# Kernel tuning notes

Measured on AMD Instinct MI355X. Metric: run time of the kernel, lower is better.

Reference implementation:

```python
import jax, jax.numpy as jnp
import numpy as np

B, L, D, H, DH, S_POKES = 1, 4096, 1024, 16, 64, 3072


def setup_inputs() -> dict:
    key = jax.random.key(0)
    k0, k1, k2, k3 = jax.random.split(key, 4)
    x = jax.random.normal(k0, (B, L, D), jnp.float32)
    pos = jax.random.uniform(k1, (B, L, 2), jnp.float32)  # positions in [0,1]^2
    qkv_w = jax.random.normal(k2, (3 * D, D), jnp.float32) * 0.02
    out_w = jax.random.normal(k3, (D, D), jnp.float32) * 0.02
    scale = jnp.ones((H,), jnp.float32) * 10.0  # per-head cosine-sim scale (init 10)
    # AxialRoPE2D freq table: logspace(pi, 10*pi), view(2, d_head//4, n_heads).mT
    n = H * DH // 4
    f = np.exp(np.linspace(np.log(np.pi), np.log(10.0 * np.pi), n + 1)[:-1])
    freqs = jnp.asarray(np.stack([f, f]).reshape(2, DH // 4, H).transpose(0, 2, 1), jnp.float32)
    return {"x": x, "pos": pos, "qkv_w": qkv_w, "out_w": out_w,
            "scale": scale, "freqs": freqs, "n_pokes": S_POKES}


def _cos_scale(q, k, scale, eps=1e-8):
    # scale_for_cosine_sim: qk logits = scale * cosine_similarity
    sq = jnp.sum(q * q, axis=-1, keepdims=True)
    sk = jnp.sum(k * k, axis=-1, keepdims=True)
    ss = jnp.sqrt(jnp.abs(scale) + eps)
    return q * (ss * jax.lax.rsqrt(sq + eps)), k * (ss * jax.lax.rsqrt(sk + eps))


def _axial_theta(pos, freqs):
    # pos [B,L,2] in [0,1]; theta [B,H,L,DH//2]
    th_w = (pos[..., None, 0:1] * 2.0 - 1.0) * freqs[0]  # [B,L,H,DH//4]
    th_h = (pos[..., None, 1:2] * 2.0 - 1.0) * freqs[1]
    return jnp.concatenate([th_h, th_w], axis=-1).transpose(0, 2, 1, 3)


def _rope(x, theta):
    d = theta.shape[-1]  # DH//2 -> rotates the full head dim, x3 part empty
    x1, x2 = x[..., :d], x[..., d:2 * d]
    cos, sin = jnp.cos(theta), jnp.sin(theta)
    return jnp.concatenate([x1 * cos - x2 * sin, x2 * cos + x1 * sin], axis=-1)


def reference(x, pos, qkv_w, out_w, scale, freqs, n_pokes):
    b, l, dm = x.shape
    qkv = x @ qkv_w.T                          # [B,L,3D]
    q, k, v = jnp.split(qkv, 3, axis=-1)
    split_heads = lambda t: t.reshape(b, l, H, DH).transpose(0, 2, 1, 3)  # [B,H,L,DH]
    q, k, v = split_heads(q), split_heads(k), split_heads(v)
    q, k = _cos_scale(q, k, scale.reshape(1, H, 1, 1))
    theta = _axial_theta(pos, freqs)
    q, k = _rope(q, theta), _rope(k, theta)
    s = n_pokes
    qp, kp, vp = q[:, :, :s], k[:, :, :s], v[:, :, :s]
    qq, kq, vq = q[:, :, s:], k[:, :, s:], v[:, :, s:]
    # pokes: causal self-attention (scale=1.0, cosine-sim logits)
    sc_pp = jnp.einsum('bhqd,bhkd->bhqk', qp, kp)
    causal = jnp.tril(jnp.ones((s, s), bool))
    p_pp = jax.nn.softmax(jnp.where(causal, sc_pp, -jnp.inf), axis=-1)
    out_p = jnp.einsum('bhqk,bhkd->bhqd', p_pp, vp)
    # queries: attend to all pokes + themselves (diagonal), never each other
    sc_qp = jnp.einsum('bhqd,bhkd->bhqk', qq, kp)          # [B,H,Q,S]
    sc_self = jnp.sum(qq * kq, axis=-1, keepdims=True)     # [B,H,Q,1]
    p_q = jax.nn.softmax(jnp.concatenate([sc_qp, sc_self], axis=-1), axis=-1)
    out_q = jnp.einsum('bhqk,bhkd->bhqd', p_q[..., :s], vp) + p_q[..., s:] * vq
    out = jnp.concatenate([out_p, out_q], axis=2).transpose(0, 2, 1, 3).reshape(b, l, dm)
    return out @ out_w.T
```

## Files before the change

### kernel.cpp

```cpp
#include <hip/hip_runtime.h>
#include <math.h>

#define SEQL   4096
#define DMODEL 1024
#define NH     16
#define DHEAD  64
#define SPOKES 3072
#define NQUERY (SEQL - SPOKES)
#define QKVN   (3 * DMODEL)

typedef short bf16x8 __attribute__((ext_vector_type(8)));
typedef short bf16x4 __attribute__((ext_vector_type(4)));
typedef float f32x4  __attribute__((ext_vector_type(4)));

__device__ __forceinline__ short f2bf(float f) {
    unsigned u = __builtin_bit_cast(unsigned, f);
    u += 0x7fffu + ((u >> 16) & 1u);
    return (short)(u >> 16);
}
__device__ __forceinline__ float bf2f(short s) {
    unsigned u = ((unsigned)(unsigned short)s) << 16;
    return __builtin_bit_cast(float, u);
}
__device__ __forceinline__ unsigned cvt_pk_bf16(float lo, float hi) {
    unsigned u;
    asm("v_cvt_pk_bf16_f32 %0, %1, %2" : "=v"(u) : "v"(lo), "v"(hi));
    return u;
}
__device__ __forceinline__ int swz(int row) { return ((row & 7) ^ (row >> 3)) << 4; }

__device__ __forceinline__ void gload_lds16(const void* g, void* l) {
    __builtin_amdgcn_global_load_lds(
        (const __attribute__((address_space(1))) unsigned int*)g,
        (__attribute__((address_space(3))) unsigned int*)l,
        16, 0, 0);
}

__global__ __launch_bounds__(256) void cvt_f32_bf16(
    const float* __restrict__ in, short* __restrict__ out, int n8)
{
    const int i = blockIdx.x * 256 + threadIdx.x;
    if (i >= n8) return;
    float4 a = ((const float4*)in)[i * 2];
    float4 b = ((const float4*)in)[i * 2 + 1];
    bf16x8 v;
    v[0] = f2bf(a.x); v[1] = f2bf(a.y); v[2] = f2bf(a.z); v[3] = f2bf(a.w);
    v[4] = f2bf(b.x); v[5] = f2bf(b.y); v[6] = f2bf(b.z); v[7] = f2bf(b.w);
    ((bf16x8*)out)[i] = v;
}

template<bool BF16OUT>
__global__ __launch_bounds__(256) void gemm_bf16(
    const short* __restrict__ A, const short* __restrict__ B, void* __restrict__ Cv,
    int K, int ldc)
{
    __shared__ short As[128 * 64];
    __shared__ short Bs[128 * 64];

    const int t = threadIdx.x;
    const int lane = t & 63, w = t >> 6;
    const int c = lane & 15, g = lane >> 4;
    const int wr = w >> 1, wc = w & 1;
    const int m0 = blockIdx.y * 128, n0 = blockIdx.x * 128;

    f32x4 acc[4][4] = {};

    for (int k0 = 0; k0 < K; k0 += 64) {
        __syncthreads();
        #pragma unroll
        for (int i = 0; i < 4; ++i) {
            const int chunk = (w * 4 + i) * 64 + lane;
            const int row = chunk >> 3, cc = chunk & 7;
            gload_lds16(A + (size_t)(m0 + row) * K + k0 + cc * 8,
                        As + (size_t)(w * 4 + i) * 512);
            gload_lds16(B + (size_t)(n0 + row) * K + k0 + cc * 8,
                        Bs + (size_t)(w * 4 + i) * 512);
        }
        __syncthreads();

        #pragma unroll
        for (int kk = 0; kk < 2; ++kk) {
            bf16x8 af[4], bf[4];
            #pragma unroll
            for (int i = 0; i < 4; ++i)
                af[i] = *(const bf16x8*)(As + (wr * 64 + i * 16 + c) * 64 + kk * 32 + g * 8);
            #pragma unroll
            for (int j = 0; j < 4; ++j)
                bf[j] = *(const bf16x8*)(Bs + (wc * 64 + j * 16 + c) * 64 + kk * 32 + g * 8);
            #pragma unroll
            for (int i = 0; i < 4; ++i)
                #pragma unroll
                for (int j = 0; j < 4; ++j)
                    acc[i][j] = __builtin_amdgcn_mfma_f32_16x16x32_bf16(af[i], bf[j], acc[i][j], 0, 0, 0);
        }
    }

    #pragma unroll
    for (int i = 0; i < 4; ++i)
        #pragma unroll
        for (int r = 0; r < 4; ++r) {
            const int row = m0 + wr * 64 + i * 16 + g * 4 + r;
            #pragma unroll
            for (int j = 0; j < 4; ++j) {
                const int col = n0 + wc * 64 + j * 16 + c;
                const float v = acc[i][j][r];
                if (BF16OUT) ((short*)Cv)[(size_t)row * ldc + col] = f2bf(v);
                else         ((float*)Cv)[(size_t)row * ldc + col] = v;
            }
        }
}

__global__ __launch_bounds__(256) void transform_qk(
    short* __restrict__ qkv, const float* __restrict__ pos,
    const float* __restrict__ scale, const float* __restrict__ freqs)
{
    const int w    = threadIdx.x >> 6;
    const int lane = threadIdx.x & 63;
    const int rid  = blockIdx.x * 4 + w;
    const int l    = rid >> 4;
    const int h    = rid & 15;

    short* qp = qkv + (size_t)l * QKVN + h * DHEAD;
    short* kp = qp + DMODEL;

    float q = bf2f(qp[lane]);
    float k = bf2f(kp[lane]);

    float sq = q * q, sk = k * k;
    #pragma unroll
    for (int o = 32; o > 0; o >>= 1) {
        sq += __shfl_xor(sq, o);
        sk += __shfl_xor(sk, o);
    }
    const float ss = sqrtf(fabsf(scale[h]) + 1e-8f);
    q *= ss * rsqrtf(sq + 1e-8f);
    k *= ss * rsqrtf(sk + 1e-8f);

    const int   j  = lane & 31;
    const float p  = pos[l * 2 + (j < 16 ? 1 : 0)];
    const float fj = (j < 16) ? freqs[256 + h * 16 + j] : freqs[h * 16 + (j - 16)];
    const float th = (p * 2.0f - 1.0f) * fj;
    const float cs = cosf(th), sn = sinf(th);

    const float qo = __shfl_xor(q, 32);
    const float ko = __shfl_xor(k, 32);
    const float qr = (lane < 32) ? q * cs - qo * sn : q * cs + qo * sn;
    const float kr = (lane < 32) ? k * cs - ko * sn : k * cs + ko * sn;

    qp[lane] = f2bf(qr);
    kp[lane] = f2bf(kr);
}

__global__ __launch_bounds__(256) void attn_fused(
    const short* __restrict__ qkv, short* __restrict__ attn,
    short* __restrict__ pacc_c, float* __restrict__ pml_c, float* __restrict__ pml0_c,
    short* __restrict__ pacc_q, float* __restrict__ pml_q, float* __restrict__ pml0_q)
{
    __shared__ short Kl[64 * 64];
    __shared__ short VTl[64 * 64];
    __shared__ short Pl[4][16 * 64];

    const int h = blockIdx.y;
    const int t = threadIdx.x, lane = t & 63, w = t >> 6;
    const int c = lane & 15, g = lane >> 4;
    const int qcol = h * DHEAD, kcol = DMODEL + h * DHEAD, vcol = 2 * DMODEL + h * DHEAD;

    const int xc = blockIdx.x;
    bool causal; int z, NS, q0, kt0, ktn, qt = 0, qb = 0;
    if (xc < 48) {
        causal = false; qb = xc / 3; z = xc - qb * 3; NS = 3;
        q0 = SPOKES + qb * 64; kt0 = z * 16; ktn = 16;
    } else {
        causal = true;
        if (xc < 96)       { const int i = xc - 48; qt = 47 - i / 3; z = i - (i / 3) * 3; NS = 3; }
        else if (xc < 128) { const int i = xc - 96; qt = 31 - (i >> 1); z = i & 1; NS = 2; }
        else               { qt = 143 - xc; z = 0; NS = 1; }
        q0 = qt * 64;
        const int full = qt + 1, b = full / NS, r = full - b * NS;
        kt0 = z * b + (z < r ? z : r);
        ktn = b + (z < r ? 1 : 0);
    }

    const int qg = q0 + w * 16 + c;

    bf16x8 qf0, qf1;
    {
        const short* qrow = qkv + (size_t)qg * QKVN + qcol;
        qf0 = *(const bf16x8*)(qrow + g * 8);
        qf1 = *(const bf16x8*)(qrow + 32 + g * 8);
    }

    float m = -INFINITY, l = 0.0f;
    f32x4 acc[4] = {};
    bf16x8 vregA, vregB;

    auto KDMA = [&](int kt) {
        const int k0 = kt * 64;
        #pragma unroll
        for (int i = 0; i < 2; ++i) {
            const int ch = i * 256 + t;
            const int kv = ch >> 3, s = ch & 7;
            const int o = s ^ ((kv & 7) ^ (kv >> 3));
            gload_lds16(qkv + (size_t)(k0 + kv) * QKVN + kcol + o * 8,
                        (char*)Kl + i * 4096 + w * 1024);
        }
    };
    auto VLOAD = [&](int kt) {
        const int k0 = kt * 64;
        const short* v0 = qkv + (size_t)(k0 + 2 * (t >> 3)) * QKVN + vcol + (t & 7) * 8;
        vregA = *(const bf16x8*)v0;
        vregB = *(const bf16x8*)(v0 + QKVN);
    };
    auto VWRITE = [&]() {
        const int p2 = t >> 3, oc = t & 7;
        #pragma unroll
        for (int j = 0; j < 8; ++j) {
            const int d = oc * 8 + j;
            const unsigned u = ((unsigned)(unsigned short)vregA[j]) |
                               (((unsigned)(unsigned short)vregB[j]) << 16);
            *(unsigned*)((char*)VTl + d * 128 + ((4 * p2) ^ swz(d))) = u;
        }
    };

    VLOAD(kt0);
    KDMA(kt0);
    VWRITE();
    __syncthreads();

    for (int it = 0; it < ktn; ++it) {
        const int kt = kt0 + it;
        const int k0 = kt * 64;

        f32x4 st[4];
        __builtin_amdgcn_s_setprio(1);
        #pragma unroll
        for (int mt = 0; mt < 4; ++mt) {
            const int kvr = mt * 16 + c;
            bf16x8 ka = *(const bf16x8*)((const char*)Kl + kvr * 128 + ((g * 16) ^ swz(kvr)));
            bf16x8 kb = *(const bf16x8*)((const char*)Kl + kvr * 128 + ((64 + g * 16) ^ swz(kvr)));
            f32x4 zz = {0.f, 0.f, 0.f, 0.f};
            zz = __builtin_amdgcn_mfma_f32_16x16x32_bf16(ka, qf0, zz, 0, 0, 0);
            st[mt] = __builtin_amdgcn_mfma_f32_16x16x32_bf16(kb, qf1, zz, 0, 0, 0);
        }
        __builtin_amdgcn_s_setprio(0);

        __syncthreads();
        if (it + 1 < ktn) { KDMA(kt + 1); VLOAD(kt + 1); }

        if (causal && (k0 + 63 > q0 + w * 16)) {
            #pragma unroll
            for (int mt = 0; mt < 4; ++mt)
                #pragma unroll
                for (int r = 0; r < 4; ++r)
                    if (k0 + mt * 16 + g * 4 + r > qg) st[mt][r] = -INFINITY;
        }
        float tmax = -INFINITY;
        #pragma unroll
        for (int mt = 0; mt < 4; ++mt)
            #pragma unroll
            for (int r = 0; r < 4; ++r) tmax = fmaxf(tmax, st[mt][r]);
        tmax = fmaxf(tmax, __shfl_xor(tmax, 16));
        tmax = fmaxf(tmax, __shfl_xor(tmax, 32));
        if (__any(tmax > m + 8.0f)) {
            const float mnew = fmaxf(m, tmax);
            const float pfac = __expf(m - mnew);
            l *= pfac;
            #pragma unroll
            for (int dt = 0; dt < 4; ++dt)
                #pragma unroll
                for (int r = 0; r < 4; ++r) acc[dt][r] *= pfac;
            m = mnew;
        }
        {
            const float mref = m;
            float rs = 0.0f;
            #pragma unroll
            for (int mt = 0; mt < 4; ++mt) {
                const float e0 = __expf(st[mt][0] - mref);
                const float e1 = __expf(st[mt][1] - mref);
                const float e2 = __expf(st[mt][2] - mref);
                const float e3 = __expf(st[mt][3] - mref);
                rs += (e0 + e1) + (e2 + e3);
                uint2 u;
                u.x = cvt_pk_bf16(e0, e1);
                u.y = cvt_pk_bf16(e2, e3);
                *(uint2*)((char*)Pl[w] + c * 128 + ((mt * 32 + g * 8) ^ swz(c))) = u;
            }
            rs += __shfl_xor(rs, 16);
            rs += __shfl_xor(rs, 32);
            l += rs;
        }

        __builtin_amdgcn_s_setprio(1);
        #pragma unroll
        for (int kc = 0; kc < 2; ++kc) {
            bf16x8 pb = *(const bf16x8*)((const char*)Pl[w] + c * 128 + ((kc * 64 + g * 16) ^ swz(c)));
            #pragma unroll
            for (int dt = 0; dt < 4; ++dt) {
                const int d = dt * 16 + c;
                bf16x8 vf = *(const bf16x8*)((const char*)VTl + d * 128 + ((kc * 64 + g * 16) ^ swz(d)));
                acc[dt] = __builtin_amdgcn_mfma_f32_16x16x32_bf16(vf, pb, acc[dt], 0, 0, 0);
            }
        }
        __builtin_amdgcn_s_setprio(0);

        __syncthreads();
        if (it + 1 < ktn) {
            VWRITE();
            __syncthreads();
        }
    }

    if (!causal && z == 0) {
        float ss = 0.0f;
        {
            const short* krow = qkv + (size_t)qg * QKVN + kcol;
            bf16x8 k0s = *(const bf16x8*)(krow + g * 8);
            bf16x8 k1s = *(const bf16x8*)(krow + 32 + g * 8);
            #pragma unroll
            for (int j = 0; j < 8; ++j)
                ss += bf2f(qf0[j]) * bf2f(k0s[j]) + bf2f(qf1[j]) * bf2f(k1s[j]);
            ss += __shfl_xor(ss, 16);
            ss += __shfl_xor(ss, 32);
        }
        const float mnew = fmaxf(m, ss);
        const float pf = __expf(m - mnew);
        const float ps = __expf(ss - mnew);
        const short* vrow = qkv + (size_t)qg * QKVN + vcol;
        #pragma unroll
        for (int dt = 0; dt < 4; ++dt) {
            bf16x4 vs = *(const bf16x4*)(vrow + dt * 16 + g * 4);
            #pragma unroll
            for (int r = 0; r < 4; ++r)
                acc[dt][r] = acc[dt][r] * pf + ps * bf2f(vs[r]);
        }
        l = l * pf + ps;
        m = mnew;
    }

    if (causal && NS == 1) {
        const float inv = 1.0f / l;
        short* orow = attn + (size_t)qg * DMODEL + qcol;
        #pragma unroll
        for (int dt = 0; dt < 4; ++dt)
            #pragma unroll
            for (int r = 0; r < 4; ++r)
                orow[dt * 16 + g * 4 + r] = f2bf(acc[dt][r] * inv);
    } else if (z == 0) {
        float* pml0 = causal ? pml0_c : pml0_q;
        const int stride = causal ? 2048 : 1024;
        const int base   = causal ? 1024 : SPOKES;
        short* orow = attn + (size_t)qg * DMODEL + qcol;
        #pragma unroll
        for (int dt = 0; dt < 4; ++dt)
            #pragma unroll
            for (int r = 0; r < 4; ++r)
                orow[dt * 16 + g * 4 + r] = f2bf(acc[dt][r]);
        if (g == 0) {
            float* p = pml0 + ((size_t)h * stride + (qg - base)) * 2;
            p[0] = m;
            p[1] = l;
        }
    } else {
        const int slot = causal ? (qt < 32 ? qt - 16 : 16 + (qt - 32) * 2 + (z - 1))
                                : qb * 2 + (z - 1);
        short* pacc = causal ? pacc_c : pacc_q;
        float* pml  = causal ? pml_c  : pml_q;
        const int rl = w * 16 + c;
        short* prow = pacc + ((size_t)slot * 64 + rl) * DMODEL + qcol;
        #pragma unroll
        for (int dt = 0; dt < 4; ++dt)
            #pragma unroll
            for (int r = 0; r < 4; ++r)
                prow[dt * 16 + g * 4 + r] = f2bf(acc[dt][r]);
        if (g == 0) {
            float* p = pml + ((size_t)(slot * 16 + h) * 64 + rl) * 2;
            p[0] = m;
            p[1] = l;
        }
    }
}

__global__ __launch_bounds__(256) void attn_combine(
    short* __restrict__ attn, const float* __restrict__ pml0,
    const short* __restrict__ pacc, const float* __restrict__ pml,
    int rowbase, int pml0_stride, int pml0_off,
    int slotBase, int slotMul, int nextra)
{
    const int i = blockIdx.x * 256 + threadIdx.x;
    const int r = i >> 7;
    const int h = (i >> 3) & 15;
    const int o = i & 7;

    const float* p0 = pml0 + ((size_t)h * pml0_stride + pml0_off + r) * 2;
    const float m0 = p0[0], l0 = p0[1];
    float M = m0;
    float me[2], le[2];
    for (int e = 0; e < nextra; ++e) {
        const int slot = slotBase + (r >> 6) * slotMul + e;
        const float* p = pml + ((size_t)(slot * 16 + h) * 64 + (r & 63)) * 2;
        me[e] = p[0]; le[e] = p[1];
        M = fmaxf(M, me[e]);
    }
    const float w0 = __expf(m0 - M);
    float L = w0 * l0;
    float we[2];
    for (int e = 0; e < nextra; ++e) { we[e] = __expf(me[e] - M); L += we[e] * le[e]; }

    short* arow = attn + (size_t)(rowbase + r) * DMODEL + h * 64 + o * 8;
    bf16x8 a0 = *(const bf16x8*)arow;
    float outv[8];
    #pragma unroll
    for (int j = 0; j < 8; ++j) outv[j] = w0 * bf2f(a0[j]);
    for (int e = 0; e < nextra; ++e) {
        const int slot = slotBase + (r >> 6) * slotMul + e;
        bf16x8 a = *(const bf16x8*)(pacc + ((size_t)slot * 64 + (r & 63)) * DMODEL + h * 64 + o * 8);
        #pragma unroll
        for (int j = 0; j < 8; ++j) outv[j] += we[e] * bf2f(a[j]);
    }
    const float inv = 1.0f / L;
    bf16x8 res;
    #pragma unroll
    for (int j = 0; j < 8; ++j) res[j] = f2bf(outv[j] * inv);
    *(bf16x8*)arow = res;
}

extern "C" void kernel_launch(void* const* d_in, const int* in_sizes, int n_in,
                              void* d_out, int out_size, void* d_ws, size_t ws_size,
                              hipStream_t stream)
{
    const float* x      = (const float*)d_in[0];
    const float* pos    = (const float*)d_in[1];
    const float* qkv_w  = (const float*)d_in[2];
    const float* out_w  = (const float*)d_in[3];
    const float* scale  = (const float*)d_in[4];
    const float* freqs  = (const float*)d_in[5];
    float*       out    = (float*)d_out;

    const size_t MB = 1024 * 1024;
    char* ws = (char*)d_ws;
    short* qkv_bf  = (short*)(ws);
    short* x_bf    = (short*)(ws + 24 * MB);
    short* wqkv_bf = (short*)(ws + 32 * MB);
    short* wout_bf = (short*)(ws + 38 * MB);
    short* pacc_c  = (short*)(ws + 40 * MB);
    float* pml_c   = (float*)(ws + 46 * MB);
    float* pml0_c  = (float*)(ws + 46 * MB + 393216);
    short* attn_bf = x_bf;
    short* pacc_q  = wqkv_bf;
    float* pml_q   = (float*)((char*)wqkv_bf + 4194304);
    float* pml0_q  = (float*)((char*)wqkv_bf + 4456448);

    const dim3 blk(256);

    cvt_f32_bf16<<<dim3(SEQL * DMODEL / 8 / 256), blk, 0, stream>>>(x, x_bf, SEQL * DMODEL / 8);
    cvt_f32_bf16<<<dim3(QKVN * DMODEL / 8 / 256), blk, 0, stream>>>(qkv_w, wqkv_bf, QKVN * DMODEL / 8);
    cvt_f32_bf16<<<dim3(DMODEL * DMODEL / 8 / 256), blk, 0, stream>>>(out_w, wout_bf, DMODEL * DMODEL / 8);

    gemm_bf16<true><<<dim3(QKVN / 128, SEQL / 128), blk, 0, stream>>>(
        x_bf, wqkv_bf, qkv_bf, DMODEL, QKVN);

    transform_qk<<<dim3(SEQL * NH / 4), blk, 0, stream>>>(qkv_bf, pos, scale, freqs);

    attn_fused<<<dim3(144, NH), blk, 0, stream>>>(
        qkv_bf, attn_bf, pacc_c, pml_c, pml0_c, pacc_q, pml_q, pml0_q);

    attn_combine<<<dim3(512), blk, 0, stream>>>(attn_bf, pml0_c, pacc_c, pml_c,
                                                1024, 2048, 0,    0, 1, 1);
    attn_combine<<<dim3(512), blk, 0, stream>>>(attn_bf, pml0_c, pacc_c, pml_c,
                                                2048, 2048, 1024, 16, 2, 2);
    attn_combine<<<dim3(512), blk, 0, stream>>>(attn_bf, pml0_q, pacc_q, pml_q,
                                                SPOKES, 1024, 0,  0, 2, 2);

    gemm_bf16<false><<<dim3(DMODEL / 128, SEQL / 128), blk, 0, stream>>>(
        attn_bf, wout_bf, out, DMODEL, DMODEL);
}
```

Before: 200.0 us.

## Use fixed softmax max from cosine-sim bound and merge cvt/combine launches

Because cosine-similarity logits are bounded by |scale|, the attention kernel replaces the online running max with a constant per-head offset. That offset is folded into the MFMA accumulator init, and log2(e) is folded into q so plain exp2 can be used. This removes the per-tile max reduction, shuffles and rescaling. Separately, the three conversion launches and the three combine launches are each merged into one. The risk is reduced numerical headroom if bf16 rounding pushes logits past the assumed bound.

```diff
diff --git a/kernel.cpp b/kernel.cpp
--- a/kernel.cpp
+++ b/kernel.cpp
@@ -8,6 +8,7 @@
 #define SPOKES 3072
 #define NQUERY (SEQL - SPOKES)
 #define QKVN   (3 * DMODEL)
+#define LOG2E  1.4426950408889634f
 
 typedef short bf16x8 __attribute__((ext_vector_type(8)));
 typedef short bf16x4 __attribute__((ext_vector_type(4)));
@@ -26,6 +27,13 @@
     unsigned u;
     asm("v_cvt_pk_bf16_f32 %0, %1, %2" : "=v"(u) : "v"(lo), "v"(hi));
     return u;
+}
+__device__ __forceinline__ float fast_exp2(float x) {
+#if __has_builtin(__builtin_amdgcn_exp2f)
+    return __builtin_amdgcn_exp2f(x);
+#else
+    float r; asm("v_exp_f32 %0, %1" : "=v"(r) : "v"(x)); return r;
+#endif
 }
 __device__ __forceinline__ int swz(int row) { return ((row & 7) ^ (row >> 3)) << 4; }
 
@@ -36,17 +44,24 @@
         16, 0, 0);
 }
 
-__global__ __launch_bounds__(256) void cvt_f32_bf16(
-    const float* __restrict__ in, short* __restrict__ out, int n8)
-{
-    const int i = blockIdx.x * 256 + threadIdx.x;
-    if (i >= n8) return;
-    float4 a = ((const float4*)in)[i * 2];
-    float4 b = ((const float4*)in)[i * 2 + 1];
+#define CVT_N0 (SEQL * DMODEL / 8)
+#define CVT_N1 (QKVN * DMODEL / 8)
+#define CVT_N2 (DMODEL * DMODEL / 8)
+__global__ __launch_bounds__(256) void cvt_all(
+    const float* __restrict__ x, const float* __restrict__ wq, const float* __restrict__ wo,
+    short* __restrict__ xb, short* __restrict__ wqb, short* __restrict__ wob)
+{
+    int i = blockIdx.x * 256 + threadIdx.x;
+    const float* src; short* dst;
+    if (i < CVT_N0)               { src = x;  dst = xb; }
+    else if (i < CVT_N0 + CVT_N1) { src = wq; dst = wqb; i -= CVT_N0; }
+    else                          { src = wo; dst = wob; i -= CVT_N0 + CVT_N1; }
+    float4 a = ((const float4*)src)[i * 2];
+    float4 b = ((const float4*)src)[i * 2 + 1];
     bf16x8 v;
     v[0] = f2bf(a.x); v[1] = f2bf(a.y); v[2] = f2bf(a.z); v[3] = f2bf(a.w);
     v[4] = f2bf(b.x); v[5] = f2bf(b.y); v[6] = f2bf(b.z); v[7] = f2bf(b.w);
-    ((bf16x8*)out)[i] = v;
+    ((bf16x8*)dst)[i] = v;
 }
 
 template<bool BF16OUT>
@@ -147,12 +162,13 @@
     const float qr = (lane < 32) ? q * cs - qo * sn : q * cs + qo * sn;
     const float kr = (lane < 32) ? k * cs - ko * sn : k * cs + ko * sn;
 
-    qp[lane] = f2bf(qr);
+    qp[lane] = f2bf(qr * LOG2E);
     kp[lane] = f2bf(kr);
 }
 
 __global__ __launch_bounds__(256) void attn_fused(
-    const short* __restrict__ qkv, short* __restrict__ attn,
+    const short* __restrict__ qkv, const float* __restrict__ scale,
+    short* __restrict__ attn,
     short* __restrict__ pacc_c, float* __restrict__ pml_c, float* __restrict__ pml0_c,
     short* __restrict__ pacc_q, float* __restrict__ pml_q, float* __restrict__ pml0_q)
 {
@@ -183,6 +199,9 @@
 
     const int qg = q0 + w * 16 + c;
 
+    const float Mlog = (fabsf(scale[h]) * 1.02f + 0.5f) * LOG2E;
+    const f32x4 negM4 = {-Mlog, -Mlog, -Mlog, -Mlog};
+
     bf16x8 qf0, qf1;
     {
         const short* qrow = qkv + (size_t)qg * QKVN + qcol;
@@ -190,7 +209,7 @@
         qf1 = *(const bf16x8*)(qrow + 32 + g * 8);
     }
 
-    float m = -INFINITY, l = 0.0f;
+    float l = 0.0f;
     f32x4 acc[4] = {};
     bf16x8 vregA, vregB;
 
@@ -238,8 +257,7 @@
             const int kvr = mt * 16 + c;
             bf16x8 ka = *(const bf16x8*)((const char*)Kl + kvr * 128 + ((g * 16) ^ swz(kvr)));
             bf16x8 kb = *(const bf16x8*)((const char*)Kl + kvr * 128 + ((64 + g * 16) ^ swz(kvr)));
-            f32x4 zz = {0.f, 0.f, 0.f, 0.f};
-            zz = __builtin_amdgcn_mfma_f32_16x16x32_bf16(ka, qf0, zz, 0, 0, 0);
+            f32x4 zz = __builtin_amdgcn_mfma_f32_16x16x32_bf16(ka, qf0, negM4, 0, 0, 0);
             st[mt] = __builtin_amdgcn_mfma_f32_16x16x32_bf16(kb, qf1, zz, 0, 0, 0);
         }
         __builtin_amdgcn_s_setprio(0);
@@ -254,32 +272,14 @@
                 for (int r = 0; r < 4; ++r)
                     if (k0 + mt * 16 + g * 4 + r > qg) st[mt][r] = -INFINITY;
         }
-        float tmax = -INFINITY;
-        #pragma unroll
-        for (int mt = 0; mt < 4; ++mt)
-            #pragma unroll
-            for (int r = 0; r < 4; ++r) tmax = fmaxf(tmax, st[mt][r]);
-        tmax = fmaxf(tmax, __shfl_xor(tmax, 16));
-        tmax = fmaxf(tmax, __shfl_xor(tmax, 32));
-        if (__any(tmax > m + 8.0f)) {
-            const float mnew = fmaxf(m, tmax);
-            const float pfac = __expf(m - mnew);
-            l *= pfac;
-            #pragma unroll
-            for (int dt = 0; dt < 4; ++dt)
-                #pragma unroll
-                for (int r = 0; r < 4; ++r) acc[dt][r] *= pfac;
-            m = mnew;
-        }
         {
-            const float mref = m;
             float rs = 0.0f;
             #pragma unroll
             for (int mt = 0; mt < 4; ++mt) {
-                const float e0 = __expf(st[mt][0] - mref);
-                const float e1 = __expf(st[mt][1] - mref);
-                const float e2 = __expf(st[mt][2] - mref);
-                const float e3 = __expf(st[mt][3] - mref);
+                const float e0 = fast_exp2(st[mt][0]);
+                const float e1 = fast_exp2(st[mt][1]);
+                const float e2 = fast_exp2(st[mt][2]);
+                const float e3 = fast_exp2(st[mt][3]);
                 rs += (e0 + e1) + (e2 + e3);
                 uint2 u;
                 u.x = cvt_pk_bf16(e0, e1);
@@ -312,30 +312,27 @@
     }
 
     if (!causal && z == 0) {
-        float ss = 0.0f;
+        float ssv = 0.0f;
         {
             const short* krow = qkv + (size_t)qg * QKVN + kcol;
             bf16x8 k0s = *(const bf16x8*)(krow + g * 8);
             bf16x8 k1s = *(const bf16x8*)(krow + 32 + g * 8);
             #pragma unroll
             for (int j = 0; j < 8; ++j)
-                ss += bf2f(qf0[j]) * bf2f(k0s[j]) + bf2f(qf1[j]) * bf2f(k1s[j]);
-            ss += __shfl_xor(ss, 16);
-            ss += __shfl_xor(ss, 32);
-        }
-        const float mnew = fmaxf(m, ss);
-        const float pf = __expf(m - mnew);
-        const float ps = __expf(ss - mnew);
+                ssv += bf2f(qf0[j]) * bf2f(k0s[j]) + bf2f(qf1[j]) * bf2f(k1s[j]);
+            ssv += __shfl_xor(ssv, 16);
+            ssv += __shfl_xor(ssv, 32);
+        }
+        const float ps = fast_exp2(ssv - Mlog);
         const short* vrow = qkv + (size_t)qg * QKVN + vcol;
         #pragma unroll
         for (int dt = 0; dt < 4; ++dt) {
             bf16x4 vs = *(const bf16x4*)(vrow + dt * 16 + g * 4);
             #pragma unroll
             for (int r = 0; r < 4; ++r)
-                acc[dt][r] = acc[dt][r] * pf + ps * bf2f(vs[r]);
-        }
-        l = l * pf + ps;
-        m = mnew;
+                acc[dt][r] += ps * bf2f(vs[r]);
+        }
+        l += ps;
     }
 
     if (causal && NS == 1) {
@@ -358,7 +355,7 @@
                 orow[dt * 16 + g * 4 + r] = f2bf(acc[dt][r]);
         if (g == 0) {
             float* p = pml0 + ((size_t)h * stride + (qg - base)) * 2;
-            p[0] = m;
+            p[0] = Mlog;
             p[1] = l;
         }
     } else {
@@ -375,22 +372,39 @@
                 prow[dt * 16 + g * 4 + r] = f2bf(acc[dt][r]);
         if (g == 0) {
             float* p = pml + ((size_t)(slot * 16 + h) * 64 + rl) * 2;
-            p[0] = m;
+            p[0] = Mlog;
             p[1] = l;
         }
     }
 }
 
-__global__ __launch_bounds__(256) void attn_combine(
-    short* __restrict__ attn, const float* __restrict__ pml0,
-    const short* __restrict__ pacc, const float* __restrict__ pml,
-    int rowbase, int pml0_stride, int pml0_off,
-    int slotBase, int slotMul, int nextra)
-{
-    const int i = blockIdx.x * 256 + threadIdx.x;
-    const int r = i >> 7;
-    const int h = (i >> 3) & 15;
-    const int o = i & 7;
+__global__ __launch_bounds__(256) void attn_combine_all(
+    short* __restrict__ attn,
+    const float* __restrict__ pml0_c, const short* __restrict__ pacc_c, const float* __restrict__ pml_c,
+    const float* __restrict__ pml0_q, const short* __restrict__ pacc_q, const float* __restrict__ pml_q)
+{
+    const int gi = blockIdx.x * 256 + threadIdx.x;
+    const int seg = gi >> 17;
+    const int li  = gi & 131071;
+    const int r = li >> 7;
+    const int h = (li >> 3) & 15;
+    const int o = li & 7;
+
+    int rowbase, pml0_stride, pml0_off, slotBase, slotMul, nextra;
+    const float* pml0; const short* pacc; const float* pml;
+    if (seg == 0) {
+        rowbase = 1024;   pml0_stride = 2048; pml0_off = 0;
+        slotBase = 0;  slotMul = 1; nextra = 1;
+        pml0 = pml0_c; pacc = pacc_c; pml = pml_c;
+    } else if (seg == 1) {
+        rowbase = 2048;   pml0_stride = 2048; pml0_off = 1024;
+        slotBase = 16; slotMul = 2; nextra = 2;
+        pml0 = pml0_c; pacc = pacc_c; pml = pml_c;
+    } else {
+        rowbase = SPOKES; pml0_stride = 1024; pml0_off = 0;
+        slotBase = 0;  slotMul = 2; nextra = 2;
+        pml0 = pml0_q; pacc = pacc_q; pml = pml_q;
+    }
 
     const float* p0 = pml0 + ((size_t)h * pml0_stride + pml0_off + r) * 2;
     const float m0 = p0[0], l0 = p0[1];
@@ -453,9 +467,8 @@
 
     const dim3 blk(256);
 
-    cvt_f32_bf16<<<dim3(SEQL * DMODEL / 8 / 256), blk, 0, stream>>>(x, x_bf, SEQL * DMODEL / 8);
-    cvt_f32_bf16<<<dim3(QKVN * DMODEL / 8 / 256), blk, 0, stream>>>(qkv_w, wqkv_bf, QKVN * DMODEL / 8);
-    cvt_f32_bf16<<<dim3(DMODEL * DMODEL / 8 / 256), blk, 0, stream>>>(out_w, wout_bf, DMODEL * DMODEL / 8);
+    cvt_all<<<dim3((CVT_N0 + CVT_N1 + CVT_N2) / 256), blk, 0, stream>>>(
+        x, qkv_w, out_w, x_bf, wqkv_bf, wout_bf);
 
     gemm_bf16<true><<<dim3(QKVN / 128, SEQL / 128), blk, 0, stream>>>(
         x_bf, wqkv_bf, qkv_bf, DMODEL, QKVN);
@@ -463,14 +476,10 @@
     transform_qk<<<dim3(SEQL * NH / 4), blk, 0, stream>>>(qkv_bf, pos, scale, freqs);
 
     attn_fused<<<dim3(144, NH), blk, 0, stream>>>(
-        qkv_bf, attn_bf, pacc_c, pml_c, pml0_c, pacc_q, pml_q, pml0_q);
-
-    attn_combine<<<dim3(512), blk, 0, stream>>>(attn_bf, pml0_c, pacc_c, pml_c,
-                                                1024, 2048, 0,    0, 1, 1);
-    attn_combine<<<dim3(512), blk, 0, stream>>>(attn_bf, pml0_c, pacc_c, pml_c,
-                                                2048, 2048, 1024, 16, 2, 2);
-    attn_combine<<<dim3(512), blk, 0, stream>>>(attn_bf, pml0_q, pacc_q, pml_q,
-                                                SPOKES, 1024, 0,  0, 2, 2);
+        qkv_bf, scale, attn_bf, pacc_c, pml_c, pml0_c, pacc_q, pml_q, pml0_q);
+
+    attn_combine_all<<<dim3(1536), blk, 0, stream>>>(
+        attn_bf, pml0_c, pacc_c, pml_c, pml0_q, pacc_q, pml_q);
 
     gemm_bf16<false><<<dim3(DMODEL / 128, SEQL / 128), blk, 0, stream>>>(
         attn_bf, wout_bf, out, DMODEL, DMODEL);
```

After: 183.8 us. -8.1%, faster.
